# Optimization experiments

Measured on AMD Instinct MI355X. Metric: run time of the kernel, lower is better.

The kernel has to match this reference:

```python
import jax, jax.numpy as jnp
import numpy as np


def setup_inputs() -> dict:
    key = jax.random.key(0)
    k1, k2, k3, k4 = jax.random.split(key, 4)
    B, T, M = 4, 2048, 1024   # batch, seq, d_model -> S = 8192 tokens
    E, F = 16, 4096           # experts (world_size*num_local_experts), d_ff
    x = jax.random.normal(k1, (B, T, M), dtype=jnp.float32) * 0.02
    Wg = jax.random.normal(k2, (M, E), dtype=jnp.float32) * 0.02
    w1 = jax.random.normal(k3, (E, M, F), dtype=jnp.float32) * 0.02
    w2 = jax.random.normal(k4, (E, F, M), dtype=jnp.float32) * 0.02
    return {"x": x, "Wg": Wg, "w1": w1, "w2": w2}


def reference(x, Wg, w1, w2):
    d = x.shape[-1]
    xr = x.reshape(-1, d)                     # (S, M)
    S = xr.shape[0]
    E = Wg.shape[1]
    C = (S + E - 1) // E                      # capacity (capacity_factor = 1.0)

    # top-1 gating (gate module = linear + softmax)
    gate = jax.nn.softmax(xr @ Wg, axis=-1)   # (S, E)
    idx = jnp.argmax(gate, axis=1)            # (S,) expert index per token
    gates_s = jnp.take_along_axis(gate, idx[:, None], axis=1)[:, 0]  # (S,)

    # cumulative-sum location within chosen expert
    onehot = jax.nn.one_hot(idx, E, dtype=jnp.int32)           # (S, E)
    loc = jnp.sum((jnp.cumsum(onehot, axis=0) - 1) * onehot, axis=1)  # (S,)
    valid = loc < C                                             # capacity drop mask

    # scatter dispatch: overflow tokens routed to a pad slot C, then sliced off
    loc_pad = jnp.minimum(loc, C)
    dispatched = jnp.zeros((E, C + 1, d), dtype=x.dtype).at[idx, loc_pad].set(xr)
    dispatched = dispatched[:, :C]            # (E, C, M)

    # all-to-all is identity (FakeAllToAllOp); per-expert FFN
    h = jax.nn.relu(jnp.einsum('ecm,emf->ecf', dispatched, w1))   # (E, C, F)
    expert_out = jnp.einsum('ecf,efm->ecm', h, w2)                # (E, C, M)

    # gather combine: rout[i] = gate_s[i] * expert_out[idx[i], loc[i]] if loc < C
    gathered = expert_out[idx, jnp.minimum(loc, C - 1)]           # (S, M)
    combined = gathered * (gates_s * valid.astype(x.dtype))[:, None]
    return combined.reshape(x.shape)
```

## Files before the change

kernel.cpp:

```cpp
#include <hip/hip_runtime.h>
#include <cstdint>
#include <cstddef>

#define S_TOK 8192
#define DM    1024
#define NE    16
#define NF    4096
#define CAP   512

typedef __attribute__((ext_vector_type(8))) short bf16x8;
typedef __attribute__((ext_vector_type(4))) float f32x4;

__device__ __forceinline__ unsigned short f2bf(float f) {
  __bf16 b = (__bf16)f;
  return __builtin_bit_cast(unsigned short, b);
}
__device__ __forceinline__ unsigned pk2(float a, float b) {
  return (unsigned)f2bf(a) | ((unsigned)f2bf(b) << 16);
}
__device__ __forceinline__ int pcol(int c) { return c ^ ((c >> 3) & 7); }

__device__ __forceinline__ void gload_lds16(const void* g, void* l) {
  __builtin_amdgcn_global_load_lds(
      (const __attribute__((address_space(1))) void*)g,
      (__attribute__((address_space(3))) void*)l, 16, 0, 0);
}

__global__ void __launch_bounds__(256)
zero_kernel(float4* __restrict__ Out, int n4) {
  const int stride = gridDim.x * 256;
  for (int i = blockIdx.x * 256 + threadIdx.x; i < n4; i += stride)
    Out[i] = float4{0.f, 0.f, 0.f, 0.f};
}

__global__ void __launch_bounds__(256)
gate_kernel(const float* __restrict__ X, const float* __restrict__ Wg,
            int* __restrict__ idx, float* __restrict__ gval) {
  const int tid  = threadIdx.x;
  const int lane = tid & 63;
  const int wid  = tid >> 6;
  const int e = lane & 15, q = lane >> 4;
  const int t0 = blockIdx.x * 16 + wid * 4;
  const int mbase = q * 256;

  const float* xp0 = X + (size_t)(t0 + 0) * DM + mbase;
  const float* xp1 = X + (size_t)(t0 + 1) * DM + mbase;
  const float* xp2 = X + (size_t)(t0 + 2) * DM + mbase;
  const float* xp3 = X + (size_t)(t0 + 3) * DM + mbase;
  const float* wp  = Wg + (size_t)mbase * NE + e;

  float a0 = 0.f, a1 = 0.f, a2 = 0.f, a3 = 0.f;
#pragma unroll 4
  for (int i = 0; i < 64; ++i) {
    float4 x0 = *(const float4*)(xp0 + i * 4);
    float4 x1 = *(const float4*)(xp1 + i * 4);
    float4 x2 = *(const float4*)(xp2 + i * 4);
    float4 x3 = *(const float4*)(xp3 + i * 4);
    float w0 = wp[(i * 4 + 0) * NE];
    float w1 = wp[(i * 4 + 1) * NE];
    float w2 = wp[(i * 4 + 2) * NE];
    float w3 = wp[(i * 4 + 3) * NE];
    a0 = fmaf(x0.x, w0, fmaf(x0.y, w1, fmaf(x0.z, w2, fmaf(x0.w, w3, a0))));
    a1 = fmaf(x1.x, w0, fmaf(x1.y, w1, fmaf(x1.z, w2, fmaf(x1.w, w3, a1))));
    a2 = fmaf(x2.x, w0, fmaf(x2.y, w1, fmaf(x2.z, w2, fmaf(x2.w, w3, a2))));
    a3 = fmaf(x3.x, w0, fmaf(x3.y, w1, fmaf(x3.z, w2, fmaf(x3.w, w3, a3))));
  }
#pragma unroll
  for (int s = 16; s < 64; s <<= 1) {
    a0 += __shfl_xor(a0, s, 64);
    a1 += __shfl_xor(a1, s, 64);
    a2 += __shfl_xor(a2, s, 64);
    a3 += __shfl_xor(a3, s, 64);
  }
  float l = (q == 0) ? a0 : (q == 1) ? a1 : (q == 2) ? a2 : a3;
  float bv = l; int bi = e;
#pragma unroll
  for (int s = 1; s < 16; s <<= 1) {
    float ov = __shfl_xor(bv, s, 16);
    int   oi = __shfl_xor(bi, s, 16);
    if (ov > bv || (ov == bv && oi < bi)) { bv = ov; bi = oi; }
  }
  float p  = expf(l - bv);
  float sm = p;
#pragma unroll
  for (int s = 1; s < 16; s <<= 1) sm += __shfl_xor(sm, s, 16);
  if (e == 0) {
    idx[t0 + q]  = bi;
    gval[t0 + q] = 1.0f / sm;
  }
}

__global__ void __launch_bounds__(1024)
scan_kernel(const int* __restrict__ idx, int* __restrict__ s2t) {
  const int tid = threadIdx.x;
#pragma unroll
  for (int k = 0; k < 8; ++k) s2t[tid + k * 1024] = -1;
  __shared__ int base[16];
  __shared__ int wavecnt[16][16];
  if (tid < 16) base[tid] = 0;
  __syncthreads();
  const int wid = tid >> 6, lane = tid & 63;
  const unsigned long long ltmask = (1ull << lane) - 1ull;
  for (int c = 0; c < 8; ++c) {
    const int t = c * 1024 + tid;
    const int e = idx[t];
    int rank = 0;
#pragma unroll
    for (int ee = 0; ee < 16; ++ee) {
      unsigned long long m = __ballot(e == ee);
      if (lane == 0) wavecnt[wid][ee] = __popcll(m);
      if (ee == e) rank = __popcll(m & ltmask);
    }
    __syncthreads();
    if (tid < 16) {
      int s = base[tid];
#pragma unroll
      for (int w = 0; w < 16; ++w) { int cc = wavecnt[w][tid]; wavecnt[w][tid] = s; s += cc; }
      base[tid] = s;
    }
    __syncthreads();
    const int loc = wavecnt[wid][e] + rank;
    if (loc < CAP) s2t[e * CAP + loc] = t;
    __syncthreads();
  }
}

__global__ void __launch_bounds__(256)
gather_kernel(const float* __restrict__ X, const int* __restrict__ s2t,
              unsigned short* __restrict__ Xg) {
  const int tid = threadIdx.x;
  const int d  = tid & 127;
  const int sl = tid >> 7;
  const int s0 = blockIdx.x * 16;
#pragma unroll 2
  for (int p = 0; p < 8; ++p) {
    const int s = s0 + p * 2 + sl;
    const int tok = s2t[s];
    uint4 w;
    if (tok >= 0) {
      const float* xp = X + (size_t)tok * DM + d * 8;
      float4 v0 = *(const float4*)xp;
      float4 v1 = *(const float4*)(xp + 4);
      w = make_uint4(pk2(v0.x, v0.y), pk2(v0.z, v0.w),
                     pk2(v1.x, v1.y), pk2(v1.z, v1.w));
    } else {
      w = make_uint4(0u, 0u, 0u, 0u);
    }
    char* dst = (char*)Xg + (size_t)(s >> 9) * 1048576 +
                (size_t)(d >> 3) * 65536 + (size_t)(d & 7) * 8192 +
                (size_t)(s & 511) * 16;
    *(uint4*)dst = w;
  }
}


#define G1_BX 2
#define G1_BY 16
#define G1_BZ 16
__global__ void __launch_bounds__(512, 2)
gemm1_kernel(const unsigned short* __restrict__ Xg, const float* __restrict__ W1,
             unsigned short* __restrict__ H2) {
  constexpr int NT = DM / 64;
  __shared__ __align__(16) char lds[131072];

  const int tid = threadIdx.x;
  const int lane = tid & 63, wid = tid >> 6;
  const int wr = wid >> 2, wc = wid & 3;
  const int ln15 = lane & 15, l16 = lane >> 4;

  const int flat = blockIdx.x + G1_BX * (blockIdx.y + G1_BY * blockIdx.z);
  const int xcd = flat & 7, jj = flat >> 3;
  const int e  = xcd * 2 + (jj >> 5);
  const int rr = jj & 31;
  const int by = rr >> 1, bx = rr & 1;
  const int m0 = bx * 256, n0 = by * 256;

  char* const Bb0 = lds + 65536;
  char* const Bb1 = lds + 98304;

  const int rb = wid >> 1;
  const int kgw = (wid & 1) * 4;
  const int adst = kgw * 4096 + rb * 1024;
  const char* const aSrc = (const char*)Xg + (size_t)e * 1048576 +
                           (size_t)(m0 + rb * 64 + lane) * 16;

  const int c0 = (tid & 63) * 4;
  const int kq = tid >> 6;
  const float* const bsrc = W1 + (size_t)e * DM * NF + (size_t)(kq * 8) * NF + n0 + c0;
  int bwoff[4];
#pragma unroll
  for (int cc = 0; cc < 4; ++cc) bwoff[cc] = kq * 4096 + pcol(c0 + cc) * 16;

  int aoff[8], boff[4];
#pragma unroll
  for (int mi = 0; mi < 8; ++mi)
    aoff[mi] = l16 * 4096 + (wr * 128 + mi * 16 + ln15) * 16;
#pragma unroll
  for (int ni = 0; ni < 4; ++ni)
    boff[ni] = l16 * 4096 + pcol(wc * 64 + ni * 16 + ln15) * 16;

  f32x4 acc[8][4];
#pragma unroll
  for (int mi = 0; mi < 8; ++mi)
#pragma unroll
    for (int ni = 0; ni < 4; ++ni) acc[mi][ni] = f32x4{0.f, 0.f, 0.f, 0.f};

  float4 breg[8];

  auto ISSUE_B = [&](int kt) {
    const float* bp = bsrc + (size_t)kt * 64 * NF;
#pragma unroll
    for (int r = 0; r < 8; ++r) breg[r] = *(const float4*)(bp + (size_t)r * NF);
  };
  auto ISSUE_A = [&](int Aoff, int kt) {
#pragma unroll
    for (int j = 0; j < 4; ++j)
      gload_lds16(aSrc + (size_t)kt * 65536 + (size_t)(kgw + j) * 8192,
                  lds + Aoff + adst + j * 4096);
  };
  auto WRITEB = [&](char* Bbuf) {
    const float* f = (const float*)breg;
#pragma unroll
    for (int cc = 0; cc < 4; ++cc)
      *(uint4*)(Bbuf + bwoff[cc]) =
          make_uint4(pk2(f[0 * 4 + cc], f[1 * 4 + cc]), pk2(f[2 * 4 + cc], f[3 * 4 + cc]),
                     pk2(f[4 * 4 + cc], f[5 * 4 + cc]), pk2(f[6 * 4 + cc], f[7 * 4 + cc]));
  };
  auto COMPUTE = [&](int Aoff, const char* Bbuf) {
#pragma unroll
    for (int kk = 0; kk < 2; ++kk) {
      bf16x8 af[8], bf[4];
#pragma unroll
      for (int mi = 0; mi < 8; ++mi)
        af[mi] = *(const bf16x8*)(lds + Aoff + kk * 16384 + aoff[mi]);
#pragma unroll
      for (int ni = 0; ni < 4; ++ni)
        bf[ni] = *(const bf16x8*)(Bbuf + kk * 16384 + boff[ni]);
      __builtin_amdgcn_s_setprio(1);
#pragma unroll
      for (int mi = 0; mi < 8; ++mi)
#pragma unroll
        for (int ni = 0; ni < 4; ++ni)
          acc[mi][ni] = __builtin_amdgcn_mfma_f32_16x16x32_bf16(af[mi], bf[ni], acc[mi][ni], 0, 0, 0);
      __builtin_amdgcn_s_setprio(0);
    }
  };

  ISSUE_A(0, 0);
  ISSUE_B(0);
  WRITEB(Bb0);
  ISSUE_B(1);
  asm volatile("s_waitcnt vmcnt(8) lgkmcnt(0)" ::: "memory");
  __builtin_amdgcn_s_barrier();

#pragma unroll 1
  for (int kt = 0; kt < NT; ++kt) {
    const int Acur = (kt & 1) ? 32768 : 0;
    const int Anxt = (kt & 1) ? 0 : 32768;
    ISSUE_A(Anxt, (kt + 1 < NT) ? kt + 1 : NT - 1);
    WRITEB((kt & 1) ? Bb0 : Bb1);
    ISSUE_B((kt + 2 < NT) ? kt + 2 : NT - 1);
    COMPUTE(Acur, (kt & 1) ? Bb1 : Bb0);
    asm volatile("s_waitcnt vmcnt(8) lgkmcnt(0)" ::: "memory");
    __builtin_amdgcn_s_barrier();
  }
  asm volatile("s_waitcnt vmcnt(0)" ::: "memory");
  __builtin_amdgcn_s_barrier();

  char* img = lds;
#pragma unroll 1
  for (int h = 0; h < 2; ++h) {
    if ((wc >> 1) == h) {
#pragma unroll
      for (int mi = 0; mi < 8; ++mi) {
#pragma unroll
        for (int ni = 0; ni < 4; ++ni) {
          const int colL = (wc & 1) * 64 + ni * 16 + ln15;
          const int basei = (colL >> 6) * 32768 + ((colL >> 3) & 7) * 4096 + (colL & 7) * 2;
#pragma unroll
          for (int j = 0; j < 4; ++j) {
            const int rowL = wr * 128 + mi * 16 + l16 * 4 + j;
            float v = acc[mi][ni][j];
            v = v > 0.f ? v : 0.f;
            *(unsigned short*)(img + basei + rowL * 16) = f2bf(v);
          }
        }
      }
    }
    __syncthreads();
    const char* src = img + tid * 128;
    char* dst = (char*)H2 + (size_t)e * 4194304 +
                (size_t)((n0 >> 6) + h * 2 + (tid >> 8)) * 65536 +
                (size_t)((tid >> 5) & 7) * 8192 +
                (size_t)(m0 + (tid & 31) * 8) * 16;
#pragma unroll
    for (int u = 0; u < 8; ++u)
      *(uint4*)(dst + u * 16) = *(const uint4*)(src + u * 16);
    __syncthreads();
  }
}

#define G2_BX 2
#define G2_BY 8
#define G2_BZ 16
__global__ void __launch_bounds__(512, 2)
gemm2_kernel(const unsigned short* __restrict__ H2, const float* __restrict__ W2,
             const int* __restrict__ s2t, const float* __restrict__ gval,
             float* __restrict__ Out) {
  constexpr int NT = NF / 64;
  __shared__ __align__(16) char lds[131072];

  const int tid = threadIdx.x;
  const int lane = tid & 63, wid = tid >> 6;
  const int wr = wid >> 1, wc = wid & 1;
  const int ln15 = lane & 15, l16 = lane >> 4;

  const int flat = blockIdx.x + G2_BX * (blockIdx.y + G2_BY * blockIdx.z);
  const int xcd = flat & 7, jj = flat >> 3;
  const int e  = xcd * 2 + (jj >> 4);
  const int rr = jj & 15;
  const int by = rr >> 1, bx = rr & 1;
  const int m0 = bx * 256, n0 = by * 128;

  char* const Bb0 = lds + 98304;
  char* const Bb1 = lds + 98304 + 16384;

  const int rb = wid >> 1;
  const int kgw = (wid & 1) * 4;
  const int adst = kgw * 4096 + rb * 1024;
  const char* const Hex = (const char*)H2 + (size_t)e * 4194304 +
                          (size_t)(m0 + rb * 64 + lane) * 16;

  const int c0 = (tid & 31) * 4;
  const int kq = tid >> 5;
  const float* const bsrc = W2 + (size_t)e * NF * DM + (size_t)(kq * 4) * DM + n0 + c0;
  const int kgb = kq >> 1, hb = kq & 1;
  int bwoff[4];
#pragma unroll
  for (int cc = 0; cc < 4; ++cc) bwoff[cc] = kgb * 2048 + pcol(c0 + cc) * 16 + hb * 8;

  int aoff[4], boff[4];
#pragma unroll
  for (int mi = 0; mi < 4; ++mi) aoff[mi] = l16 * 4096 + (wr * 64 + mi * 16 + ln15) * 16;
#pragma unroll
  for (int ni = 0; ni < 4; ++ni) boff[ni] = l16 * 2048 + pcol(wc * 64 + ni * 16 + ln15) * 16;

  f32x4 acc[4][4];
#pragma unroll
  for (int mi = 0; mi < 4; ++mi)
#pragma unroll
    for (int ni = 0; ni < 4; ++ni) acc[mi][ni] = f32x4{0.f, 0.f, 0.f, 0.f};

  float4 breg[4];

  auto ISSUE_B = [&](int kt) {
    const float* bp = bsrc + (size_t)kt * 64 * DM;
#pragma unroll
    for (int r = 0; r < 4; ++r) breg[r] = *(const float4*)(bp + (size_t)r * DM);
  };
  auto ISSUE_A = [&](int Aoff, int kt) {
#pragma unroll
    for (int j = 0; j < 4; ++j)
      gload_lds16(Hex + (size_t)kt * 65536 + (size_t)(kgw + j) * 8192,
                  lds + Aoff + adst + j * 4096);
  };
  auto WRITEB = [&](char* Bbuf) {
    const float* f = (const float*)breg;
#pragma unroll
    for (int cc = 0; cc < 4; ++cc)
      *(uint2*)(Bbuf + bwoff[cc]) =
          make_uint2(pk2(f[0 + cc], f[4 + cc]), pk2(f[8 + cc], f[12 + cc]));
  };
  auto COMPUTE = [&](int Aoff, const char* Bbuf) {
#pragma unroll
    for (int kk = 0; kk < 2; ++kk) {
      bf16x8 af[4], bf[4];
#pragma unroll
      for (int mi = 0; mi < 4; ++mi)
        af[mi] = *(const bf16x8*)(lds + Aoff + kk * 16384 + aoff[mi]);
#pragma unroll
      for (int ni = 0; ni < 4; ++ni)
        bf[ni] = *(const bf16x8*)(Bbuf + kk * 8192 + boff[ni]);
#pragma unroll
      for (int mi = 0; mi < 4; ++mi)
#pragma unroll
        for (int ni = 0; ni < 4; ++ni)
          acc[mi][ni] = __builtin_amdgcn_mfma_f32_16x16x32_bf16(af[mi], bf[ni], acc[mi][ni], 0, 0, 0);
    }
  };

  ISSUE_B(0); ISSUE_A(0, 0);
  WRITEB(Bb0);
  ISSUE_B(1); ISSUE_A(32768, 1);
  asm volatile("s_waitcnt vmcnt(8) lgkmcnt(0)" ::: "memory");
  __builtin_amdgcn_s_barrier();

  int aCur = 0, aNxt = 32768, aNx2 = 65536;
  for (int kt = 0; kt < NT; ++kt) {
    WRITEB((kt & 1) ? Bb0 : Bb1);
    const int tl = (kt + 2 < NT) ? kt + 2 : NT - 1;
    ISSUE_B(tl);
    ISSUE_A(aNx2, tl);
    COMPUTE(aCur, (kt & 1) ? Bb1 : Bb0);
    asm volatile("s_waitcnt vmcnt(8) lgkmcnt(0)" ::: "memory");
    __builtin_amdgcn_s_barrier();
    const int t = aCur; aCur = aNxt; aNxt = aNx2; aNx2 = t;
  }
  asm volatile("s_waitcnt vmcnt(0)" ::: "memory");

#pragma unroll
  for (int mi = 0; mi < 4; ++mi) {
#pragma unroll
    for (int ni = 0; ni < 4; ++ni) {
      const int col = n0 + wc * 64 + ni * 16 + ln15;
#pragma unroll
      for (int j = 0; j < 4; ++j) {
        const int row = m0 + wr * 64 + mi * 16 + l16 * 4 + j;
        const int tk = s2t[e * CAP + row];
        if (tk >= 0)
          Out[(size_t)tk * DM + col] = acc[mi][ni][j] * gval[tk];
      }
    }
  }
}

extern "C" void kernel_launch(void* const* d_in, const int* in_sizes, int n_in,
                              void* d_out, int out_size, void* d_ws, size_t ws_size,
                              hipStream_t stream) {
  (void)in_sizes; (void)n_in; (void)ws_size;
  const float* X  = (const float*)d_in[0];
  const float* Wg = (const float*)d_in[1];
  const float* W1 = (const float*)d_in[2];
  const float* W2 = (const float*)d_in[3];
  float* Out = (float*)d_out;

  char* ws = (char*)d_ws;
  int*   s2t  = (int*)ws;
  int*   idx  = (int*)(ws + 32768);
  float* gval = (float*)(ws + 65536);
  unsigned short* Xg = (unsigned short*)(ws + 98304);
  unsigned short* H2 = (unsigned short*)(ws + 98304 + 16777216);

  zero_kernel<<<2048, 256, 0, stream>>>((float4*)Out, out_size / 4);
  gate_kernel<<<S_TOK / 16, 256, 0, stream>>>(X, Wg, idx, gval);
  scan_kernel<<<1, 1024, 0, stream>>>(idx, s2t);
  gather_kernel<<<512, 256, 0, stream>>>(X, s2t, Xg);
  gemm1_kernel<<<dim3(G1_BX, G1_BY, G1_BZ), 512, 0, stream>>>(Xg, W1, H2);
  gemm2_kernel<<<dim3(G2_BX, G2_BY, G2_BZ), 512, 0, stream>>>(H2, W2, s2t, gval, Out);
}
```

Before: 281.0 us.

## Split GEMM main loops into four barrier-synchronized phases interleaving loads with MFMA

Both expert GEMM kernels now run each K-tile as four quadrant phases. Each phase reads its A/B fragments from LDS, issues one slice of the next tile's global loads or the LDS B-write, then hits a barrier before the MFMA block. The goal is to spread memory traffic across the compute and keep waves in lockstep, in the style of ping-pong scheduling. gemm2 drops from triple to double buffering for A and uses less LDS, and both kernels drop the min-blocks hint from launch_bounds. The extra barriers add sync overhead, and dropping the occupancy hint may raise register use and lower occupancy.

```diff
diff --git a/kernel.cpp b/kernel.cpp
--- a/kernel.cpp
+++ b/kernel.cpp
@@ -157,7 +157,7 @@
 #define G1_BX 2
 #define G1_BY 16
 #define G1_BZ 16
-__global__ void __launch_bounds__(512, 2)
+__global__ void __launch_bounds__(512)
 gemm1_kernel(const unsigned short* __restrict__ Xg, const float* __restrict__ W1,
              unsigned short* __restrict__ H2) {
   constexpr int NT = DM / 64;
@@ -212,11 +212,11 @@
 #pragma unroll
     for (int r = 0; r < 8; ++r) breg[r] = *(const float4*)(bp + (size_t)r * NF);
   };
-  auto ISSUE_A = [&](int Aoff, int kt) {
-#pragma unroll
-    for (int j = 0; j < 4; ++j)
-      gload_lds16(aSrc + (size_t)kt * 65536 + (size_t)(kgw + j) * 8192,
-                  lds + Aoff + adst + j * 4096);
+  auto ISSUE_A2 = [&](int Aoff, int kt, int j0) {
+#pragma unroll
+    for (int j = 0; j < 2; ++j)
+      gload_lds16(aSrc + (size_t)kt * 65536 + (size_t)(kgw + j0 + j) * 8192,
+                  lds + Aoff + adst + (j0 + j) * 4096);
   };
   auto WRITEB = [&](char* Bbuf) {
     const float* f = (const float*)breg;
@@ -226,42 +226,56 @@
           make_uint4(pk2(f[0 * 4 + cc], f[1 * 4 + cc]), pk2(f[2 * 4 + cc], f[3 * 4 + cc]),
                      pk2(f[4 * 4 + cc], f[5 * 4 + cc]), pk2(f[6 * 4 + cc], f[7 * 4 + cc]));
   };
-  auto COMPUTE = [&](int Aoff, const char* Bbuf) {
+  auto PHASE = [&](int Aoff, const char* Bbuf, int mh, int nh, auto issue) {
+    bf16x8 a[8], b[4];
 #pragma unroll
     for (int kk = 0; kk < 2; ++kk) {
-      bf16x8 af[8], bf[4];
-#pragma unroll
-      for (int mi = 0; mi < 8; ++mi)
-        af[mi] = *(const bf16x8*)(lds + Aoff + kk * 16384 + aoff[mi]);
-#pragma unroll
-      for (int ni = 0; ni < 4; ++ni)
-        bf[ni] = *(const bf16x8*)(Bbuf + kk * 16384 + boff[ni]);
-      __builtin_amdgcn_s_setprio(1);
-#pragma unroll
-      for (int mi = 0; mi < 8; ++mi)
-#pragma unroll
-        for (int ni = 0; ni < 4; ++ni)
-          acc[mi][ni] = __builtin_amdgcn_mfma_f32_16x16x32_bf16(af[mi], bf[ni], acc[mi][ni], 0, 0, 0);
-      __builtin_amdgcn_s_setprio(0);
-    }
-  };
-
-  ISSUE_A(0, 0);
+#pragma unroll
+      for (int i = 0; i < 4; ++i)
+        a[kk * 4 + i] = *(const bf16x8*)(lds + Aoff + kk * 16384 + aoff[mh * 4 + i]);
+#pragma unroll
+      for (int j = 0; j < 2; ++j)
+        b[kk * 2 + j] = *(const bf16x8*)(Bbuf + kk * 16384 + boff[nh * 2 + j]);
+    }
+    issue();
+    __builtin_amdgcn_s_barrier();
+    asm volatile("s_waitcnt lgkmcnt(0)" ::: "memory");
+    __builtin_amdgcn_sched_barrier(0);
+    __builtin_amdgcn_s_setprio(1);
+#pragma unroll
+    for (int kk = 0; kk < 2; ++kk)
+#pragma unroll
+      for (int i = 0; i < 4; ++i)
+#pragma unroll
+        for (int j = 0; j < 2; ++j)
+          acc[mh * 4 + i][nh * 2 + j] = __builtin_amdgcn_mfma_f32_16x16x32_bf16(
+              a[kk * 4 + i], b[kk * 2 + j], acc[mh * 4 + i][nh * 2 + j], 0, 0, 0);
+    __builtin_amdgcn_s_setprio(0);
+  };
+
+  ISSUE_A2(0, 0, 0); ISSUE_A2(0, 0, 2);
   ISSUE_B(0);
   WRITEB(Bb0);
   ISSUE_B(1);
-  asm volatile("s_waitcnt vmcnt(8) lgkmcnt(0)" ::: "memory");
+  asm volatile("s_waitcnt lgkmcnt(0)" ::: "memory");
   __builtin_amdgcn_s_barrier();
 
 #pragma unroll 1
   for (int kt = 0; kt < NT; ++kt) {
     const int Acur = (kt & 1) ? 32768 : 0;
-    const int Anxt = (kt & 1) ? 0 : 32768;
-    ISSUE_A(Anxt, (kt + 1 < NT) ? kt + 1 : NT - 1);
-    WRITEB((kt & 1) ? Bb0 : Bb1);
-    ISSUE_B((kt + 2 < NT) ? kt + 2 : NT - 1);
-    COMPUTE(Acur, (kt & 1) ? Bb1 : Bb0);
-    asm volatile("s_waitcnt vmcnt(8) lgkmcnt(0)" ::: "memory");
+    const int Anxt = Acur ^ 32768;
+    char* const Bcur = (kt & 1) ? Bb1 : Bb0;
+    char* const Bnxt = (kt & 1) ? Bb0 : Bb1;
+    const int ka = (kt + 1 < NT) ? kt + 1 : NT - 1;
+    const int kb = (kt + 2 < NT) ? kt + 2 : NT - 1;
+    PHASE(Acur, Bcur, 0, 0, [&] { ISSUE_A2(Anxt, ka, 0); });
+    __builtin_amdgcn_s_barrier();
+    PHASE(Acur, Bcur, 0, 1, [&] { ISSUE_A2(Anxt, ka, 2); });
+    __builtin_amdgcn_s_barrier();
+    PHASE(Acur, Bcur, 1, 0, [&] { WRITEB(Bnxt); });
+    __builtin_amdgcn_s_barrier();
+    PHASE(Acur, Bcur, 1, 1, [&] { ISSUE_B(kb); });
+    asm volatile("s_waitcnt vmcnt(8)" ::: "memory");
     __builtin_amdgcn_s_barrier();
   }
   asm volatile("s_waitcnt vmcnt(0)" ::: "memory");
@@ -303,12 +317,12 @@
 #define G2_BX 2
 #define G2_BY 8
 #define G2_BZ 16
-__global__ void __launch_bounds__(512, 2)
+__global__ void __launch_bounds__(512)
 gemm2_kernel(const unsigned short* __restrict__ H2, const float* __restrict__ W2,
              const int* __restrict__ s2t, const float* __restrict__ gval,
              float* __restrict__ Out) {
   constexpr int NT = NF / 64;
-  __shared__ __align__(16) char lds[131072];
+  __shared__ __align__(16) char lds[98304];
 
   const int tid = threadIdx.x;
   const int lane = tid & 63, wid = tid >> 6;
@@ -322,14 +336,14 @@
   const int by = rr >> 1, bx = rr & 1;
   const int m0 = bx * 256, n0 = by * 128;
 
-  char* const Bb0 = lds + 98304;
-  char* const Bb1 = lds + 98304 + 16384;
+  char* const Bb0 = lds + 65536;
+  char* const Bb1 = lds + 81920;
 
   const int rb = wid >> 1;
   const int kgw = (wid & 1) * 4;
   const int adst = kgw * 4096 + rb * 1024;
-  const char* const Hex = (const char*)H2 + (size_t)e * 4194304 +
-                          (size_t)(m0 + rb * 64 + lane) * 16;
+  const char* const aSrc = (const char*)H2 + (size_t)e * 4194304 +
+                           (size_t)(m0 + rb * 64 + lane) * 16;
 
   const int c0 = (tid & 31) * 4;
   const int kq = tid >> 5;
@@ -358,11 +372,11 @@
 #pragma unroll
     for (int r = 0; r < 4; ++r) breg[r] = *(const float4*)(bp + (size_t)r * DM);
   };
-  auto ISSUE_A = [&](int Aoff, int kt) {
-#pragma unroll
-    for (int j = 0; j < 4; ++j)
-      gload_lds16(Hex + (size_t)kt * 65536 + (size_t)(kgw + j) * 8192,
-                  lds + Aoff + adst + j * 4096);
+  auto ISSUE_A2 = [&](int Aoff, int kt, int j0) {
+#pragma unroll
+    for (int j = 0; j < 2; ++j)
+      gload_lds16(aSrc + (size_t)kt * 65536 + (size_t)(kgw + j0 + j) * 8192,
+                  lds + Aoff + adst + (j0 + j) * 4096);
   };
   auto WRITEB = [&](char* Bbuf) {
     const float* f = (const float*)breg;
@@ -371,40 +385,57 @@
       *(uint2*)(Bbuf + bwoff[cc]) =
           make_uint2(pk2(f[0 + cc], f[4 + cc]), pk2(f[8 + cc], f[12 + cc]));
   };
-  auto COMPUTE = [&](int Aoff, const char* Bbuf) {
+  auto PHASE = [&](int Aoff, const char* Bbuf, int mh, int nh, auto issue) {
+    bf16x8 a[4], b[4];
 #pragma unroll
     for (int kk = 0; kk < 2; ++kk) {
-      bf16x8 af[4], bf[4];
-#pragma unroll
-      for (int mi = 0; mi < 4; ++mi)
-        af[mi] = *(const bf16x8*)(lds + Aoff + kk * 16384 + aoff[mi]);
-#pragma unroll
-      for (int ni = 0; ni < 4; ++ni)
-        bf[ni] = *(const bf16x8*)(Bbuf + kk * 8192 + boff[ni]);
-#pragma unroll
-      for (int mi = 0; mi < 4; ++mi)
-#pragma unroll
-        for (int ni = 0; ni < 4; ++ni)
-          acc[mi][ni] = __builtin_amdgcn_mfma_f32_16x16x32_bf16(af[mi], bf[ni], acc[mi][ni], 0, 0, 0);
-    }
-  };
-
-  ISSUE_B(0); ISSUE_A(0, 0);
+#pragma unroll
+      for (int i = 0; i < 2; ++i)
+        a[kk * 2 + i] = *(const bf16x8*)(lds + Aoff + kk * 16384 + aoff[mh * 2 + i]);
+#pragma unroll
+      for (int j = 0; j < 2; ++j)
+        b[kk * 2 + j] = *(const bf16x8*)(Bbuf + kk * 8192 + boff[nh * 2 + j]);
+    }
+    issue();
+    __builtin_amdgcn_s_barrier();
+    asm volatile("s_waitcnt lgkmcnt(0)" ::: "memory");
+    __builtin_amdgcn_sched_barrier(0);
+    __builtin_amdgcn_s_setprio(1);
+#pragma unroll
+    for (int kk = 0; kk < 2; ++kk)
+#pragma unroll
+      for (int i = 0; i < 2; ++i)
+#pragma unroll
+        for (int j = 0; j < 2; ++j)
+          acc[mh * 2 + i][nh * 2 + j] = __builtin_amdgcn_mfma_f32_16x16x32_bf16(
+              a[kk * 2 + i], b[kk * 2 + j], acc[mh * 2 + i][nh * 2 + j], 0, 0, 0);
+    __builtin_amdgcn_s_setprio(0);
+  };
+
+  ISSUE_A2(0, 0, 0); ISSUE_A2(0, 0, 2);
+  ISSUE_B(0);
   WRITEB(Bb0);
-  ISSUE_B(1); ISSUE_A(32768, 1);
-  asm volatile("s_waitcnt vmcnt(8) lgkmcnt(0)" ::: "memory");
+  ISSUE_B(1);
+  asm volatile("s_waitcnt lgkmcnt(0)" ::: "memory");
   __builtin_amdgcn_s_barrier();
 
-  int aCur = 0, aNxt = 32768, aNx2 = 65536;
+#pragma unroll 1
   for (int kt = 0; kt < NT; ++kt) {
-    WRITEB((kt & 1) ? Bb0 : Bb1);
-    const int tl = (kt + 2 < NT) ? kt + 2 : NT - 1;
-    ISSUE_B(tl);
-    ISSUE_A(aNx2, tl);
-    COMPUTE(aCur, (kt & 1) ? Bb1 : Bb0);
-    asm volatile("s_waitcnt vmcnt(8) lgkmcnt(0)" ::: "memory");
-    __builtin_amdgcn_s_barrier();
-    const int t = aCur; aCur = aNxt; aNxt = aNx2; aNx2 = t;
+    const int Acur = (kt & 1) ? 32768 : 0;
+    const int Anxt = Acur ^ 32768;
+    char* const Bcur = (kt & 1) ? Bb1 : Bb0;
+    char* const Bnxt = (kt & 1) ? Bb0 : Bb1;
+    const int ka = (kt + 1 < NT) ? kt + 1 : NT - 1;
+    const int kb = (kt + 2 < NT) ? kt + 2 : NT - 1;
+    PHASE(Acur, Bcur, 0, 0, [&] { ISSUE_A2(Anxt, ka, 0); });
+    __builtin_amdgcn_s_barrier();
+    PHASE(Acur, Bcur, 0, 1, [&] { ISSUE_A2(Anxt, ka, 2); });
+    __builtin_amdgcn_s_barrier();
+    PHASE(Acur, Bcur, 1, 0, [&] { WRITEB(Bnxt); });
+    __builtin_amdgcn_s_barrier();
+    PHASE(Acur, Bcur, 1, 1, [&] { ISSUE_B(kb); });
+    asm volatile("s_waitcnt vmcnt(4)" ::: "memory");
+    __builtin_amdgcn_s_barrier();
   }
   asm volatile("s_waitcnt vmcnt(0)" ::: "memory");
 
```

After: 314.8 us. 1.12x slower.
